# Optimization experiments

Hardware: AMD Instinct MI355X
Metric: run time of the kernel (lower is better)

## Reference

```python
import jax, jax.numpy as jnp
import numpy as np

N = 50000
E = 800000
D = 128
O = 128


def _spmm_coo(rows, cols, vals, x, n_rows):
    # out[r] += vals[e] * x[cols[e]]  (COO sparse matrix times dense matrix)
    gathered = vals[:, None] * x[cols]            # [E, O]
    return jax.ops.segment_sum(gathered, rows, num_segments=n_rows)


def setup_inputs() -> dict:
    key = jax.random.key(0)
    ks = jax.random.split(key, 9)
    return {
        "inputs": jax.random.normal(ks[0], (N, D), dtype=jnp.float32),
        "adj1_rows": jax.random.randint(ks[1], (E,), 0, N, dtype=jnp.int32),
        "adj1_cols": jax.random.randint(ks[2], (E,), 0, N, dtype=jnp.int32),
        "adj1_vals": jax.random.uniform(ks[3], (E,), dtype=jnp.float32),
        "adj2_rows": jax.random.randint(ks[4], (E,), 0, N, dtype=jnp.int32),
        "adj2_cols": jax.random.randint(ks[5], (E,), 0, N, dtype=jnp.int32),
        "adj2_vals": jax.random.uniform(ks[6], (E,), dtype=jnp.float32),
        "weights_1": jax.random.normal(ks[7], (D, O), dtype=jnp.float32) * (6.0 / (D + O)) ** 0.5,
        "weights_2": jax.random.normal(ks[8], (D, O), dtype=jnp.float32) * (6.0 / (D + O)) ** 0.5,
    }


def reference(inputs, adj1_rows, adj1_cols, adj1_vals,
              adj2_rows, adj2_cols, adj2_vals, weights_1, weights_2):
    # dense projection per relation
    x1 = inputs @ weights_1                        # [N, O]
    x2 = inputs @ weights_2                        # [N, O]
    # sparse aggregation per relation
    y1 = _spmm_coo(adj1_rows, adj1_cols, adj1_vals, x1, N)
    y2 = _spmm_coo(adj2_rows, adj2_cols, adj2_vals, x2, N)
    return jax.nn.relu(y1 + y2)
```

## Files before the change

kernel.cpp:

```cpp
#include <hip/hip_runtime.h>


typedef __attribute__((ext_vector_type(4))) float     f32x4;
typedef __attribute__((ext_vector_type(8))) short     bf16x8;

#define NB      782
#define BSLOTS  10
#define BCAP    2560
#define SCAP    64

static __device__ __forceinline__ unsigned short f2bf(float f) {
    unsigned u = __float_as_uint(f);
    u += 0x7FFF + ((u >> 16) & 1);
    return (unsigned short)(u >> 16);
}

__global__ __launch_bounds__(256) void convert_kernel(
    const float* __restrict__ X,
    const float* __restrict__ W1, const float* __restrict__ W2,
    unsigned short* __restrict__ Xb, unsigned short* __restrict__ Wt, int n)
{
    const int stride = gridDim.x * blockDim.x;
    const int nW = 2 * 128 * 128;
    const int nX = n * 32;
    const int total = nW + nX;
    for (int g = blockIdx.x * blockDim.x + threadIdx.x; g < total; g += stride) {
        if (g < nW) {
            const int rel = g >> 14;
            const int o   = (g >> 7) & 127;
            const int k   = g & 127;
            const float* W = rel ? W2 : W1;
            Wt[g] = f2bf(W[k * 128 + o]);
        } else {
            const int i = g - nW;
            const float4 v = ((const float4*)X)[i];
            ushort4 b;
            b.x = f2bf(v.x); b.y = f2bf(v.y); b.z = f2bf(v.z); b.w = f2bf(v.w);
            ((ushort4*)Xb)[i] = b;
        }
    }
}

__global__ __launch_bounds__(256) void bin_kernel(
    const int* __restrict__ rows1, const int* __restrict__ cols1, const float* __restrict__ vals1,
    const int* __restrict__ rows2, const int* __restrict__ cols2, const float* __restrict__ vals2,
    int* __restrict__ gcur, unsigned long long* __restrict__ edges_tmp,
    int E, int n)
{
    __shared__ unsigned long long stage[NB][BSLOTS];
    __shared__ int scnt[NB];

    for (int i = threadIdx.x; i < NB; i += 256) scnt[i] = 0;
    __syncthreads();

    const int stride = gridDim.x * 256;
    const int total  = 2 * E;
    for (int g = blockIdx.x * 256 + threadIdx.x; g < total; g += stride) {
        int r, col, rel; float v;
        if (g < E) { r = rows1[g]; col = cols1[g]; rel = 0; v = vals1[g]; }
        else       { int e = g - E; r = rows2[e]; col = cols2[e]; rel = 1; v = vals2[e]; }

        const int b = r >> 6;
        const unsigned lo = (unsigned)(r & 63) | ((unsigned)rel << 6) | ((unsigned)col << 7);
        const unsigned long long pack =
            (unsigned long long)lo | ((unsigned long long)__float_as_uint(v) << 32);

        const int pos = atomicAdd(&scnt[b], 1);
        if (pos < BSLOTS) {
            stage[b][pos] = pack;
        } else {
            int gp = atomicAdd(&gcur[b], 1);
            if (gp < BCAP) edges_tmp[(size_t)b * BCAP + gp] = pack;
        }
    }
    __syncthreads();

    for (int b = threadIdx.x; b < NB; b += 256) {
        int k = scnt[b]; if (k > BSLOTS) k = BSLOTS;
        if (k > 0) {
            int base = atomicAdd(&gcur[b], k);
            for (int i = 0; i < k; ++i)
                if (base + i < BCAP)
                    edges_tmp[(size_t)b * BCAP + base + i] = stage[b][i];
        }
    }
}

__global__ __launch_bounds__(256) void agg_kernel(
    const int* __restrict__ gcur,
    const unsigned long long* __restrict__ edges_tmp,
    const unsigned short* __restrict__ Xb,
    unsigned short* __restrict__ agg, int n)
{
    __shared__ unsigned long long lists[32 * SCAP];
    __shared__ int cnt[32];

    const int nwg = NB * 4;
    const int xcd = blockIdx.x & 7, bi = blockIdx.x >> 3;
    const int q8 = nwg >> 3;
    const int swz = xcd * q8 + bi;

    const int b   = swz >> 2;
    const int q   = swz & 3;
    const int tid = threadIdx.x;
    const int rowbase = b * 64 + q * 16;
    if (rowbase >= n) return;

    int sz = gcur[b]; if (sz > BCAP) sz = BCAP;
    const unsigned long long* ebase = edges_tmp + (size_t)b * BCAP;

    if (tid < 32) cnt[tid] = 0;
    __syncthreads();

    for (int e = tid; e < sz; e += 256) {
        const unsigned long long p = ebase[e];
        const unsigned lo = (unsigned)p;
        const int rl = (int)(lo & 63u);
        if ((rl >> 4) == q) {
            const int seg = ((rl & 15) << 1) | ((lo >> 6) & 1);
            const int pos = atomicAdd(&cnt[seg], 1);
            if (pos < SCAP) lists[seg * SCAP + pos] = p;
        }
    }
    __syncthreads();

    const int lane = tid & 31;
    const int grp  = tid >> 5;
    for (int seg = grp; seg < 32; seg += 8) {
        const int row = rowbase + (seg >> 1);
        if (row >= n) continue;
        const int rel = seg & 1;
        int m = cnt[seg]; if (m > SCAP) m = SCAP;
        const unsigned long long* lst = &lists[seg * SCAP];
        float4 acc = make_float4(0.f, 0.f, 0.f, 0.f);

        int e = 0;
        for (; e + 4 <= m; e += 4) {
            const unsigned long long p0 = lst[e + 0];
            const unsigned long long p1 = lst[e + 1];
            const unsigned long long p2 = lst[e + 2];
            const unsigned long long p3 = lst[e + 3];
            const ushort4 x0 = *(const ushort4*)&Xb[(size_t)(((unsigned)p0 >> 7) & 0xFFFFu) * 128 + lane * 4];
            const ushort4 x1 = *(const ushort4*)&Xb[(size_t)(((unsigned)p1 >> 7) & 0xFFFFu) * 128 + lane * 4];
            const ushort4 x2 = *(const ushort4*)&Xb[(size_t)(((unsigned)p2 >> 7) & 0xFFFFu) * 128 + lane * 4];
            const ushort4 x3 = *(const ushort4*)&Xb[(size_t)(((unsigned)p3 >> 7) & 0xFFFFu) * 128 + lane * 4];
            const float v0 = __uint_as_float((unsigned)(p0 >> 32));
            const float v1 = __uint_as_float((unsigned)(p1 >> 32));
            const float v2 = __uint_as_float((unsigned)(p2 >> 32));
            const float v3 = __uint_as_float((unsigned)(p3 >> 32));
            acc.x = fmaf(v0, __uint_as_float((unsigned)x0.x << 16), acc.x);
            acc.y = fmaf(v0, __uint_as_float((unsigned)x0.y << 16), acc.y);
            acc.z = fmaf(v0, __uint_as_float((unsigned)x0.z << 16), acc.z);
            acc.w = fmaf(v0, __uint_as_float((unsigned)x0.w << 16), acc.w);
            acc.x = fmaf(v1, __uint_as_float((unsigned)x1.x << 16), acc.x);
            acc.y = fmaf(v1, __uint_as_float((unsigned)x1.y << 16), acc.y);
            acc.z = fmaf(v1, __uint_as_float((unsigned)x1.z << 16), acc.z);
            acc.w = fmaf(v1, __uint_as_float((unsigned)x1.w << 16), acc.w);
            acc.x = fmaf(v2, __uint_as_float((unsigned)x2.x << 16), acc.x);
            acc.y = fmaf(v2, __uint_as_float((unsigned)x2.y << 16), acc.y);
            acc.z = fmaf(v2, __uint_as_float((unsigned)x2.z << 16), acc.z);
            acc.w = fmaf(v2, __uint_as_float((unsigned)x2.w << 16), acc.w);
            acc.x = fmaf(v3, __uint_as_float((unsigned)x3.x << 16), acc.x);
            acc.y = fmaf(v3, __uint_as_float((unsigned)x3.y << 16), acc.y);
            acc.z = fmaf(v3, __uint_as_float((unsigned)x3.z << 16), acc.z);
            acc.w = fmaf(v3, __uint_as_float((unsigned)x3.w << 16), acc.w);
        }
        for (; e < m; ++e) {
            const unsigned long long p = lst[e];
            const ushort4 xv = *(const ushort4*)&Xb[(size_t)(((unsigned)p >> 7) & 0xFFFFu) * 128 + lane * 4];
            const float v  = __uint_as_float((unsigned)(p >> 32));
            acc.x = fmaf(v, __uint_as_float((unsigned)xv.x << 16), acc.x);
            acc.y = fmaf(v, __uint_as_float((unsigned)xv.y << 16), acc.y);
            acc.z = fmaf(v, __uint_as_float((unsigned)xv.z << 16), acc.z);
            acc.w = fmaf(v, __uint_as_float((unsigned)xv.w << 16), acc.w);
        }

        ushort4 o;
        o.x = f2bf(acc.x); o.y = f2bf(acc.y); o.z = f2bf(acc.z); o.w = f2bf(acc.w);
        *(ushort4*)&agg[((size_t)rel * n + row) * 128 + lane * 4] = o;
    }
}

__global__ __launch_bounds__(256) void gemm_relu_kernel(
    const unsigned short* __restrict__ agg,
    const unsigned short* __restrict__ Wt,
    float* __restrict__ out, int n)
{
    const int lane = threadIdx.x & 63;
    const int w    = threadIdx.x >> 6;
    const int colbase = w * 32;
    const int l15 = lane & 15;
    const int lhi = lane >> 4;

    bf16x8 bfrag[2][2][4];
    #pragma unroll
    for (int rel = 0; rel < 2; ++rel) {
        const unsigned short* Wr = Wt + rel * 16384;
        #pragma unroll
        for (int ct = 0; ct < 2; ++ct) {
            const int o = colbase + ct * 16 + l15;
            #pragma unroll
            for (int ks = 0; ks < 4; ++ks)
                bfrag[rel][ct][ks] = *(const bf16x8*)&Wr[o * 128 + ks * 32 + lhi * 8];
        }
    }

    const int row0 = blockIdx.x * 32;
    const f32x4 zero = {0.f, 0.f, 0.f, 0.f};

    #pragma unroll
    for (int rt = 0; rt < 2; ++rt) {
        const int r0 = row0 + rt * 16;
        int ra = r0 + l15; if (ra >= n) ra = n - 1;
        bf16x8 af0[4], af1[4];
        #pragma unroll
        for (int ks = 0; ks < 4; ++ks) {
            af0[ks] = *(const bf16x8*)&agg[(size_t)ra * 128 + ks * 32 + lhi * 8];
            af1[ks] = *(const bf16x8*)&agg[((size_t)n + ra) * 128 + ks * 32 + lhi * 8];
        }

        f32x4 acc[2];
        acc[0] = zero; acc[1] = zero;
        #pragma unroll
        for (int ks = 0; ks < 4; ++ks) {
            acc[0] = __builtin_amdgcn_mfma_f32_16x16x32_bf16(af0[ks], bfrag[0][0][ks], acc[0], 0, 0, 0);
            acc[1] = __builtin_amdgcn_mfma_f32_16x16x32_bf16(af0[ks], bfrag[0][1][ks], acc[1], 0, 0, 0);
            acc[0] = __builtin_amdgcn_mfma_f32_16x16x32_bf16(af1[ks], bfrag[1][0][ks], acc[0], 0, 0, 0);
            acc[1] = __builtin_amdgcn_mfma_f32_16x16x32_bf16(af1[ks], bfrag[1][1][ks], acc[1], 0, 0, 0);
        }

        #pragma unroll
        for (int ct = 0; ct < 2; ++ct) {
            const int col = colbase + ct * 16 + l15;
            #pragma unroll
            for (int j = 0; j < 4; ++j) {
                const int r = r0 + lhi * 4 + j;
                if (r < n) out[(size_t)r * 128 + col] = fmaxf(acc[ct][j], 0.f);
            }
        }
    }
}

extern "C" void kernel_launch(void* const* d_in, const int* in_sizes, int n_in,
                              void* d_out, int out_size, void* d_ws, size_t ws_size,
                              hipStream_t stream)
{
    const float* X  = (const float*)d_in[0];
    const int*   r1 = (const int*)  d_in[1];
    const int*   c1 = (const int*)  d_in[2];
    const float* v1 = (const float*)d_in[3];
    const int*   r2 = (const int*)  d_in[4];
    const int*   c2 = (const int*)  d_in[5];
    const float* v2 = (const float*)d_in[6];
    const float* W1 = (const float*)d_in[7];
    const float* W2 = (const float*)d_in[8];
    float*       out = (float*)d_out;

    const int n = in_sizes[0] / 128;
    const int E = in_sizes[1];

    unsigned short* agg = (unsigned short*)d_ws;
    unsigned short* Xb  = agg + (size_t)2 * n * 128;
    unsigned short* Wt  = Xb + (size_t)n * 128;
    unsigned long long* edges_tmp =
        (unsigned long long*)(((uintptr_t)(Wt + 2 * 128 * 128) + 255) & ~(uintptr_t)255);
    int* gcur = (int*)(edges_tmp + (size_t)NB * BCAP);

    hipMemsetAsync(gcur, 0, NB * sizeof(int), stream);

    convert_kernel<<<2048, 256, 0, stream>>>(X, W1, W2, Xb, Wt, n);

    bin_kernel<<<512, 256, 0, stream>>>(r1, c1, v1, r2, c2, v2, gcur, edges_tmp, E, n);

    agg_kernel<<<NB * 4, 256, 0, stream>>>(gcur, edges_tmp, Xb, agg, n);

    gemm_relu_kernel<<<(n + 31) / 32, 256, 0, stream>>>(agg, Wt, out, n);
}
```

Baseline: 129.8 us.

## Two-pass radix binning of edges, fused convert, and persistent atomic-queue aggregation

Replaces the single-pass binning into 782 row buckets with two passes. The first pass buckets edges into 13 super-bins of 4096 rows, with relation 0 filling from the front and relation 1 from the back of each region, and it shares one launch with the bf16 conversion. A second kernel then splits each super-bin into 64-row buckets through larger shared-memory staging. This is meant to cut the global atomics and scattered writes caused by tiny per-block staging. The aggregation kernel becomes persistent and takes 16-row chunks from a global atomic counter. This adds an extra pass over the edge list and reuses the agg workspace as scratch for the super-bins.

```diff
diff --git a/kernel.cpp b/kernel.cpp
--- a/kernel.cpp
+++ b/kernel.cpp
@@ -5,9 +5,14 @@
 typedef __attribute__((ext_vector_type(8))) short     bf16x8;
 
 #define NB      782
-#define BSLOTS  10
+#define NSUP    13
+#define SB1     64
+#define SCAPS   147456
+#define B2BLK   79
 #define BCAP    2560
 #define SCAP    64
+#define BIN1G   2048
+#define CONVG   256
 
 static __device__ __forceinline__ unsigned short f2bf(float f) {
     unsigned u = __float_as_uint(f);
@@ -15,169 +20,248 @@
     return (unsigned short)(u >> 16);
 }
 
-__global__ __launch_bounds__(256) void convert_kernel(
+__global__ __launch_bounds__(256) void convbin1_kernel(
     const float* __restrict__ X,
     const float* __restrict__ W1, const float* __restrict__ W2,
-    unsigned short* __restrict__ Xb, unsigned short* __restrict__ Wt, int n)
-{
-    const int stride = gridDim.x * blockDim.x;
-    const int nW = 2 * 128 * 128;
-    const int nX = n * 32;
-    const int total = nW + nX;
-    for (int g = blockIdx.x * blockDim.x + threadIdx.x; g < total; g += stride) {
-        if (g < nW) {
-            const int rel = g >> 14;
-            const int o   = (g >> 7) & 127;
-            const int k   = g & 127;
-            const float* W = rel ? W2 : W1;
-            Wt[g] = f2bf(W[k * 128 + o]);
-        } else {
-            const int i = g - nW;
-            const float4 v = ((const float4*)X)[i];
-            ushort4 b;
-            b.x = f2bf(v.x); b.y = f2bf(v.y); b.z = f2bf(v.z); b.w = f2bf(v.w);
-            ((ushort4*)Xb)[i] = b;
-        }
-    }
-}
-
-__global__ __launch_bounds__(256) void bin_kernel(
     const int* __restrict__ rows1, const int* __restrict__ cols1, const float* __restrict__ vals1,
     const int* __restrict__ rows2, const int* __restrict__ cols2, const float* __restrict__ vals2,
-    int* __restrict__ gcur, unsigned long long* __restrict__ edges_tmp,
+    unsigned short* __restrict__ Xb, unsigned short* __restrict__ Wt,
+    int* __restrict__ gcur1, unsigned long long* __restrict__ super_tmp,
     int E, int n)
 {
-    __shared__ unsigned long long stage[NB][BSLOTS];
-    __shared__ int scnt[NB];
-
-    for (int i = threadIdx.x; i < NB; i += 256) scnt[i] = 0;
+    if (blockIdx.x >= BIN1G) {
+        const int stride = CONVG * 256;
+        const int nW = 2 * 128 * 128;
+        const int nX = n * 32;
+        const int total = nW + nX;
+        for (int g = (blockIdx.x - BIN1G) * 256 + threadIdx.x; g < total; g += stride) {
+            if (g < nW) {
+                const int rel = g >> 14;
+                const int o   = (g >> 7) & 127;
+                const int k   = g & 127;
+                const float* W = rel ? W2 : W1;
+                Wt[g] = f2bf(W[k * 128 + o]);
+            } else {
+                const int i = g - nW;
+                const float4 v = ((const float4*)X)[i];
+                ushort4 b;
+                b.x = f2bf(v.x); b.y = f2bf(v.y); b.z = f2bf(v.z); b.w = f2bf(v.w);
+                ((ushort4*)Xb)[i] = b;
+            }
+        }
+        return;
+    }
+
+    __shared__ unsigned long long stage[2 * NSUP][SB1];
+    __shared__ int scnt[2 * NSUP];
+
+    for (int i = threadIdx.x; i < 2 * NSUP; i += 256) scnt[i] = 0;
     __syncthreads();
 
-    const int stride = gridDim.x * 256;
-    const int total  = 2 * E;
-    for (int g = blockIdx.x * 256 + threadIdx.x; g < total; g += stride) {
+    const int total = 2 * E;
+    for (int g = blockIdx.x * 256 + threadIdx.x; g < total; g += BIN1G * 256) {
         int r, col, rel; float v;
         if (g < E) { r = rows1[g]; col = cols1[g]; rel = 0; v = vals1[g]; }
         else       { int e = g - E; r = rows2[e]; col = cols2[e]; rel = 1; v = vals2[e]; }
 
-        const int b = r >> 6;
-        const unsigned lo = (unsigned)(r & 63) | ((unsigned)rel << 6) | ((unsigned)col << 7);
+        const int s   = r >> 12;
+        const int key = s * 2 + rel;
         const unsigned long long pack =
-            (unsigned long long)lo | ((unsigned long long)__float_as_uint(v) << 32);
-
-        const int pos = atomicAdd(&scnt[b], 1);
-        if (pos < BSLOTS) {
-            stage[b][pos] = pack;
+            (unsigned long long)((unsigned)(r & 0xFFFF) | ((unsigned)col << 16))
+            | ((unsigned long long)__float_as_uint(v) << 32);
+
+        const int pos = atomicAdd(&scnt[key], 1);
+        if (pos < SB1) {
+            stage[key][pos] = pack;
         } else {
-            int gp = atomicAdd(&gcur[b], 1);
-            if (gp < BCAP) edges_tmp[(size_t)b * BCAP + gp] = pack;
+            if (rel == 0) {
+                int gp = atomicAdd(&gcur1[2 * s], 1);
+                if (gp < SCAPS) super_tmp[(size_t)s * SCAPS + gp] = pack;
+            } else {
+                int gp = atomicAdd(&gcur1[2 * s + 1], 1);
+                if (gp < SCAPS) super_tmp[(size_t)s * SCAPS + (SCAPS - 1 - gp)] = pack;
+            }
         }
     }
     __syncthreads();
 
-    for (int b = threadIdx.x; b < NB; b += 256) {
-        int k = scnt[b]; if (k > BSLOTS) k = BSLOTS;
+    for (int key = threadIdx.x; key < 2 * NSUP; key += 256) {
+        int k = scnt[key]; if (k > SB1) k = SB1;
         if (k > 0) {
-            int base = atomicAdd(&gcur[b], k);
-            for (int i = 0; i < k; ++i)
-                if (base + i < BCAP)
-                    edges_tmp[(size_t)b * BCAP + base + i] = stage[b][i];
-        }
+            const int s = key >> 1, rel = key & 1;
+            if (rel == 0) {
+                int base = atomicAdd(&gcur1[2 * s], k);
+                for (int i = 0; i < k; ++i) {
+                    int gp = base + i;
+                    if (gp < SCAPS) super_tmp[(size_t)s * SCAPS + gp] = stage[key][i];
+                }
+            } else {
+                int base = atomicAdd(&gcur1[2 * s + 1], k);
+                for (int i = 0; i < k; ++i) {
+                    int gp = base + i;
+                    if (gp < SCAPS) super_tmp[(size_t)s * SCAPS + (SCAPS - 1 - gp)] = stage[key][i];
+                }
+            }
+        }
+    }
+}
+
+__global__ __launch_bounds__(256) void bin2_kernel(
+    const int* __restrict__ gcur1,
+    const unsigned long long* __restrict__ super_tmp,
+    int* __restrict__ gcur2, unsigned long long* __restrict__ edges_tmp,
+    int n)
+{
+    __shared__ unsigned long long stage[64][32];
+    __shared__ int scnt[64];
+
+    const int s  = blockIdx.x / B2BLK;
+    const int bi = blockIdx.x % B2BLK;
+    const int tid = threadIdx.x;
+
+    for (int i = tid; i < 64; i += 256) scnt[i] = 0;
+    __syncthreads();
+
+    int lo = gcur1[2 * s];     if (lo > SCAPS) lo = SCAPS;
+    int hi = gcur1[2 * s + 1]; if (hi > SCAPS) hi = SCAPS;
+    const unsigned long long* reg = super_tmp + (size_t)s * SCAPS;
+
+    #pragma unroll
+    for (int rel = 0; rel < 2; ++rel) {
+        const int cnt = rel ? hi : lo;
+        for (int k = bi * 256 + tid; k < cnt; k += B2BLK * 256) {
+            const unsigned long long p = rel ? reg[SCAPS - 1 - k] : reg[k];
+            const unsigned lo32 = (unsigned)p;
+            const int row = (int)(lo32 & 0xFFFFu);
+            const int col = (int)(lo32 >> 16);
+            const unsigned long long pack =
+                (unsigned long long)((unsigned)(row & 63) | ((unsigned)rel << 6) | ((unsigned)col << 7))
+                | (p & 0xFFFFFFFF00000000ull);
+
+            const int bl  = (row >> 6) & 63;
+            const int pos = atomicAdd(&scnt[bl], 1);
+            if (pos < 32) {
+                stage[bl][pos] = pack;
+            } else {
+                const int b = row >> 6;
+                int gp = atomicAdd(&gcur2[b], 1);
+                if (gp < BCAP) edges_tmp[(size_t)b * BCAP + gp] = pack;
+            }
+        }
+        __syncthreads();
+        for (int bl = tid; bl < 64; bl += 256) {
+            int k = scnt[bl]; if (k > 32) k = 32;
+            if (k > 0) {
+                const int b = (s << 6) + bl;
+                int base = atomicAdd(&gcur2[b], k);
+                for (int i = 0; i < k; ++i)
+                    if (base + i < BCAP)
+                        edges_tmp[(size_t)b * BCAP + base + i] = stage[bl][i];
+            }
+            scnt[bl] = 0;
+        }
+        __syncthreads();
     }
 }
 
 __global__ __launch_bounds__(256) void agg_kernel(
-    const int* __restrict__ gcur,
+    const int* __restrict__ gcur2,
     const unsigned long long* __restrict__ edges_tmp,
     const unsigned short* __restrict__ Xb,
-    unsigned short* __restrict__ agg, int n)
+    unsigned short* __restrict__ agg,
+    int* __restrict__ wctr, int n)
 {
     __shared__ unsigned long long lists[32 * SCAP];
     __shared__ int cnt[32];
-
-    const int nwg = NB * 4;
-    const int xcd = blockIdx.x & 7, bi = blockIdx.x >> 3;
-    const int q8 = nwg >> 3;
-    const int swz = xcd * q8 + bi;
-
-    const int b   = swz >> 2;
-    const int q   = swz & 3;
+    __shared__ int chunk_s;
+
     const int tid = threadIdx.x;
-    const int rowbase = b * 64 + q * 16;
-    if (rowbase >= n) return;
-
-    int sz = gcur[b]; if (sz > BCAP) sz = BCAP;
-    const unsigned long long* ebase = edges_tmp + (size_t)b * BCAP;
-
-    if (tid < 32) cnt[tid] = 0;
-    __syncthreads();
-
-    for (int e = tid; e < sz; e += 256) {
-        const unsigned long long p = ebase[e];
-        const unsigned lo = (unsigned)p;
-        const int rl = (int)(lo & 63u);
-        if ((rl >> 4) == q) {
-            const int seg = ((rl & 15) << 1) | ((lo >> 6) & 1);
-            const int pos = atomicAdd(&cnt[seg], 1);
-            if (pos < SCAP) lists[seg * SCAP + pos] = p;
-        }
-    }
-    __syncthreads();
-
-    const int lane = tid & 31;
-    const int grp  = tid >> 5;
-    for (int seg = grp; seg < 32; seg += 8) {
-        const int row = rowbase + (seg >> 1);
-        if (row >= n) continue;
-        const int rel = seg & 1;
-        int m = cnt[seg]; if (m > SCAP) m = SCAP;
-        const unsigned long long* lst = &lists[seg * SCAP];
-        float4 acc = make_float4(0.f, 0.f, 0.f, 0.f);
-
-        int e = 0;
-        for (; e + 4 <= m; e += 4) {
-            const unsigned long long p0 = lst[e + 0];
-            const unsigned long long p1 = lst[e + 1];
-            const unsigned long long p2 = lst[e + 2];
-            const unsigned long long p3 = lst[e + 3];
-            const ushort4 x0 = *(const ushort4*)&Xb[(size_t)(((unsigned)p0 >> 7) & 0xFFFFu) * 128 + lane * 4];
-            const ushort4 x1 = *(const ushort4*)&Xb[(size_t)(((unsigned)p1 >> 7) & 0xFFFFu) * 128 + lane * 4];
-            const ushort4 x2 = *(const ushort4*)&Xb[(size_t)(((unsigned)p2 >> 7) & 0xFFFFu) * 128 + lane * 4];
-            const ushort4 x3 = *(const ushort4*)&Xb[(size_t)(((unsigned)p3 >> 7) & 0xFFFFu) * 128 + lane * 4];
-            const float v0 = __uint_as_float((unsigned)(p0 >> 32));
-            const float v1 = __uint_as_float((unsigned)(p1 >> 32));
-            const float v2 = __uint_as_float((unsigned)(p2 >> 32));
-            const float v3 = __uint_as_float((unsigned)(p3 >> 32));
-            acc.x = fmaf(v0, __uint_as_float((unsigned)x0.x << 16), acc.x);
-            acc.y = fmaf(v0, __uint_as_float((unsigned)x0.y << 16), acc.y);
-            acc.z = fmaf(v0, __uint_as_float((unsigned)x0.z << 16), acc.z);
-            acc.w = fmaf(v0, __uint_as_float((unsigned)x0.w << 16), acc.w);
-            acc.x = fmaf(v1, __uint_as_float((unsigned)x1.x << 16), acc.x);
-            acc.y = fmaf(v1, __uint_as_float((unsigned)x1.y << 16), acc.y);
-            acc.z = fmaf(v1, __uint_as_float((unsigned)x1.z << 16), acc.z);
-            acc.w = fmaf(v1, __uint_as_float((unsigned)x1.w << 16), acc.w);
-            acc.x = fmaf(v2, __uint_as_float((unsigned)x2.x << 16), acc.x);
-            acc.y = fmaf(v2, __uint_as_float((unsigned)x2.y << 16), acc.y);
-            acc.z = fmaf(v2, __uint_as_float((unsigned)x2.z << 16), acc.z);
-            acc.w = fmaf(v2, __uint_as_float((unsigned)x2.w << 16), acc.w);
-            acc.x = fmaf(v3, __uint_as_float((unsigned)x3.x << 16), acc.x);
-            acc.y = fmaf(v3, __uint_as_float((unsigned)x3.y << 16), acc.y);
-            acc.z = fmaf(v3, __uint_as_float((unsigned)x3.z << 16), acc.z);
-            acc.w = fmaf(v3, __uint_as_float((unsigned)x3.w << 16), acc.w);
-        }
-        for (; e < m; ++e) {
-            const unsigned long long p = lst[e];
-            const ushort4 xv = *(const ushort4*)&Xb[(size_t)(((unsigned)p >> 7) & 0xFFFFu) * 128 + lane * 4];
-            const float v  = __uint_as_float((unsigned)(p >> 32));
-            acc.x = fmaf(v, __uint_as_float((unsigned)xv.x << 16), acc.x);
-            acc.y = fmaf(v, __uint_as_float((unsigned)xv.y << 16), acc.y);
-            acc.z = fmaf(v, __uint_as_float((unsigned)xv.z << 16), acc.z);
-            acc.w = fmaf(v, __uint_as_float((unsigned)xv.w << 16), acc.w);
-        }
-
-        ushort4 o;
-        o.x = f2bf(acc.x); o.y = f2bf(acc.y); o.z = f2bf(acc.z); o.w = f2bf(acc.w);
-        *(ushort4*)&agg[((size_t)rel * n + row) * 128 + lane * 4] = o;
+    const int NQ = (n + 15) >> 4;
+
+    for (;;) {
+        __syncthreads();
+        if (tid == 0) chunk_s = atomicAdd(wctr, 1);
+        __syncthreads();
+        const int c = chunk_s;
+        if (c >= NQ) return;
+
+        const int b = c >> 2;
+        const int q = c & 3;
+        const int rowbase = c * 16;
+
+        int sz = gcur2[b]; if (sz > BCAP) sz = BCAP;
+        const unsigned long long* ebase = edges_tmp + (size_t)b * BCAP;
+
+        if (tid < 32) cnt[tid] = 0;
+        __syncthreads();
+
+        for (int e = tid; e < sz; e += 256) {
+            const unsigned long long p = ebase[e];
+            const unsigned lo = (unsigned)p;
+            const int rl = (int)(lo & 63u);
+            if ((rl >> 4) == q) {
+                const int seg = ((rl & 15) << 1) | ((lo >> 6) & 1);
+                const int pos = atomicAdd(&cnt[seg], 1);
+                if (pos < SCAP) lists[seg * SCAP + pos] = p;
+            }
+        }
+        __syncthreads();
+
+        const int lane = tid & 31;
+        const int grp  = tid >> 5;
+        for (int seg = grp; seg < 32; seg += 8) {
+            const int row = rowbase + (seg >> 1);
+            if (row >= n) continue;
+            const int rel = seg & 1;
+            int m = cnt[seg]; if (m > SCAP) m = SCAP;
+            const unsigned long long* lst = &lists[seg * SCAP];
+            float4 acc = make_float4(0.f, 0.f, 0.f, 0.f);
+
+            int e = 0;
+            for (; e + 4 <= m; e += 4) {
+                const unsigned long long p0 = lst[e + 0];
+                const unsigned long long p1 = lst[e + 1];
+                const unsigned long long p2 = lst[e + 2];
+                const unsigned long long p3 = lst[e + 3];
+                const ushort4 x0 = *(const ushort4*)&Xb[(size_t)(((unsigned)p0 >> 7) & 0xFFFFu) * 128 + lane * 4];
+                const ushort4 x1 = *(const ushort4*)&Xb[(size_t)(((unsigned)p1 >> 7) & 0xFFFFu) * 128 + lane * 4];
+                const ushort4 x2 = *(const ushort4*)&Xb[(size_t)(((unsigned)p2 >> 7) & 0xFFFFu) * 128 + lane * 4];
+                const ushort4 x3 = *(const ushort4*)&Xb[(size_t)(((unsigned)p3 >> 7) & 0xFFFFu) * 128 + lane * 4];
+                const float v0 = __uint_as_float((unsigned)(p0 >> 32));
+                const float v1 = __uint_as_float((unsigned)(p1 >> 32));
+                const float v2 = __uint_as_float((unsigned)(p2 >> 32));
+                const float v3 = __uint_as_float((unsigned)(p3 >> 32));
+                acc.x = fmaf(v0, __uint_as_float((unsigned)x0.x << 16), acc.x);
+                acc.y = fmaf(v0, __uint_as_float((unsigned)x0.y << 16), acc.y);
+                acc.z = fmaf(v0, __uint_as_float((unsigned)x0.z << 16), acc.z);
+                acc.w = fmaf(v0, __uint_as_float((unsigned)x0.w << 16), acc.w);
+                acc.x = fmaf(v1, __uint_as_float((unsigned)x1.x << 16), acc.x);
+                acc.y = fmaf(v1, __uint_as_float((unsigned)x1.y << 16), acc.y);
+                acc.z = fmaf(v1, __uint_as_float((unsigned)x1.z << 16), acc.z);
+                acc.w = fmaf(v1, __uint_as_float((unsigned)x1.w << 16), acc.w);
+                acc.x = fmaf(v2, __uint_as_float((unsigned)x2.x << 16), acc.x);
+                acc.y = fmaf(v2, __uint_as_float((unsigned)x2.y << 16), acc.y);
+                acc.z = fmaf(v2, __uint_as_float((unsigned)x2.z << 16), acc.z);
+                acc.w = fmaf(v2, __uint_as_float((unsigned)x2.w << 16), acc.w);
+                acc.x = fmaf(v3, __uint_as_float((unsigned)x3.x << 16), acc.x);
+                acc.y = fmaf(v3, __uint_as_float((unsigned)x3.y << 16), acc.y);
+                acc.z = fmaf(v3, __uint_as_float((unsigned)x3.z << 16), acc.z);
+                acc.w = fmaf(v3, __uint_as_float((unsigned)x3.w << 16), acc.w);
+            }
+            for (; e < m; ++e) {
+                const unsigned long long p = lst[e];
+                const ushort4 xv = *(const ushort4*)&Xb[(size_t)(((unsigned)p >> 7) & 0xFFFFu) * 128 + lane * 4];
+                const float v  = __uint_as_float((unsigned)(p >> 32));
+                acc.x = fmaf(v, __uint_as_float((unsigned)xv.x << 16), acc.x);
+                acc.y = fmaf(v, __uint_as_float((unsigned)xv.y << 16), acc.y);
+                acc.z = fmaf(v, __uint_as_float((unsigned)xv.z << 16), acc.z);
+                acc.w = fmaf(v, __uint_as_float((unsigned)xv.w << 16), acc.w);
+            }
+
+            ushort4 o;
+            o.x = f2bf(acc.x); o.y = f2bf(acc.y); o.z = f2bf(acc.z); o.w = f2bf(acc.w);
+            *(ushort4*)&agg[((size_t)rel * n + row) * 128 + lane * 4] = o;
+        }
     }
 }
 
@@ -260,19 +344,23 @@
     const int E = in_sizes[1];
 
     unsigned short* agg = (unsigned short*)d_ws;
+    unsigned long long* super_tmp = (unsigned long long*)d_ws;
     unsigned short* Xb  = agg + (size_t)2 * n * 128;
     unsigned short* Wt  = Xb + (size_t)n * 128;
     unsigned long long* edges_tmp =
         (unsigned long long*)(((uintptr_t)(Wt + 2 * 128 * 128) + 255) & ~(uintptr_t)255);
-    int* gcur = (int*)(edges_tmp + (size_t)NB * BCAP);
-
-    hipMemsetAsync(gcur, 0, NB * sizeof(int), stream);
-
-    convert_kernel<<<2048, 256, 0, stream>>>(X, W1, W2, Xb, Wt, n);
-
-    bin_kernel<<<512, 256, 0, stream>>>(r1, c1, v1, r2, c2, v2, gcur, edges_tmp, E, n);
-
-    agg_kernel<<<NB * 4, 256, 0, stream>>>(gcur, edges_tmp, Xb, agg, n);
+    int* gcur1 = (int*)(edges_tmp + (size_t)NB * BCAP);
+    int* gcur2 = gcur1 + 2 * NSUP;
+    int* wctr  = gcur2 + NB;
+
+    hipMemsetAsync(gcur1, 0, (2 * NSUP + NB + 1) * sizeof(int), stream);
+
+    convbin1_kernel<<<BIN1G + CONVG, 256, 0, stream>>>(
+        X, W1, W2, r1, c1, v1, r2, c2, v2, Xb, Wt, gcur1, super_tmp, E, n);
+
+    bin2_kernel<<<NSUP * B2BLK, 256, 0, stream>>>(gcur1, super_tmp, gcur2, edges_tmp, n);
+
+    agg_kernel<<<2048, 256, 0, stream>>>(gcur2, edges_tmp, Xb, agg, wctr, n);
 
     gemm_relu_kernel<<<(n + 31) / 32, 256, 0, stream>>>(agg, Wt, out, n);
 }
```

Result: slower. 194.8 us (+50.1%).

## Fuse convert and bin kernels, split bins by half, shrink agg tiles to 8 rows

Applied to the files above, without the earlier changes.

Merges the bf16 conversion and edge binning into one launch, where dedicated blocks do the conversion while the rest bin edges. The binning blocks now work in pairs: each pair reads a contiguous slice of edges and each block keeps only rows in its half of the bins, which halves shared staging per block and allows more staging slots. The aggregation kernel now processes 8 rows per workgroup instead of 16, doubling the grid, with an XCD-aware swizzle that handles a remainder. The intent is to overlap conversion with binning, drop a launch, and raise parallelism in aggregation, at the cost of each edge being read twice and more redundant bin scans in aggregation.

```diff
diff --git a/kernel.cpp b/kernel.cpp
--- a/kernel.cpp
+++ b/kernel.cpp
@@ -5,9 +5,12 @@
 typedef __attribute__((ext_vector_type(8))) short     bf16x8;
 
 #define NB      782
-#define BSLOTS  10
+#define NBH     391
+#define BSLOTS  12
 #define BCAP    2560
 #define SCAP    64
+#define BING    512
+#define CONVG   256
 
 static __device__ __forceinline__ unsigned short f2bf(float f) {
     unsigned u = __float_as_uint(f);
@@ -15,59 +18,70 @@
     return (unsigned short)(u >> 16);
 }
 
-__global__ __launch_bounds__(256) void convert_kernel(
+__global__ __launch_bounds__(256) void convbin_kernel(
     const float* __restrict__ X,
     const float* __restrict__ W1, const float* __restrict__ W2,
-    unsigned short* __restrict__ Xb, unsigned short* __restrict__ Wt, int n)
-{
-    const int stride = gridDim.x * blockDim.x;
-    const int nW = 2 * 128 * 128;
-    const int nX = n * 32;
-    const int total = nW + nX;
-    for (int g = blockIdx.x * blockDim.x + threadIdx.x; g < total; g += stride) {
-        if (g < nW) {
-            const int rel = g >> 14;
-            const int o   = (g >> 7) & 127;
-            const int k   = g & 127;
-            const float* W = rel ? W2 : W1;
-            Wt[g] = f2bf(W[k * 128 + o]);
-        } else {
-            const int i = g - nW;
-            const float4 v = ((const float4*)X)[i];
-            ushort4 b;
-            b.x = f2bf(v.x); b.y = f2bf(v.y); b.z = f2bf(v.z); b.w = f2bf(v.w);
-            ((ushort4*)Xb)[i] = b;
-        }
-    }
-}
-
-__global__ __launch_bounds__(256) void bin_kernel(
     const int* __restrict__ rows1, const int* __restrict__ cols1, const float* __restrict__ vals1,
     const int* __restrict__ rows2, const int* __restrict__ cols2, const float* __restrict__ vals2,
+    unsigned short* __restrict__ Xb, unsigned short* __restrict__ Wt,
     int* __restrict__ gcur, unsigned long long* __restrict__ edges_tmp,
     int E, int n)
 {
-    __shared__ unsigned long long stage[NB][BSLOTS];
-    __shared__ int scnt[NB];
-
-    for (int i = threadIdx.x; i < NB; i += 256) scnt[i] = 0;
-    __syncthreads();
-
-    const int stride = gridDim.x * 256;
-    const int total  = 2 * E;
-    for (int g = blockIdx.x * 256 + threadIdx.x; g < total; g += stride) {
+    if (blockIdx.x >= BING) {
+        const int stride = CONVG * 256;
+        const int nW = 2 * 128 * 128;
+        const int nX = n * 32;
+        const int total = nW + nX;
+        for (int g = (blockIdx.x - BING) * 256 + threadIdx.x; g < total; g += stride) {
+            if (g < nW) {
+                const int rel = g >> 14;
+                const int o   = (g >> 7) & 127;
+                const int k   = g & 127;
+                const float* W = rel ? W2 : W1;
+                Wt[g] = f2bf(W[k * 128 + o]);
+            } else {
+                const int i = g - nW;
+                const float4 v = ((const float4*)X)[i];
+                ushort4 b;
+                b.x = f2bf(v.x); b.y = f2bf(v.y); b.z = f2bf(v.z); b.w = f2bf(v.w);
+                ((ushort4*)Xb)[i] = b;
+            }
+        }
+        return;
+    }
+
+    __shared__ unsigned long long stage[NBH][BSLOTS];
+    __shared__ int scnt[NBH];
+
+    const int slice = blockIdx.x >> 1;
+    const int half  = blockIdx.x & 1;
+    const int tid   = threadIdx.x;
+
+    for (int i = tid; i < NBH; i += 256) scnt[i] = 0;
+    __syncthreads();
+
+    const int total = 2 * E;
+    const int per   = (total + (BING / 2) - 1) / (BING / 2);
+    const int base  = slice * per;
+    const int end   = min(base + per, total);
+
+    for (int g = base + tid; g < end; g += 256) {
         int r, col, rel; float v;
         if (g < E) { r = rows1[g]; col = cols1[g]; rel = 0; v = vals1[g]; }
         else       { int e = g - E; r = rows2[e]; col = cols2[e]; rel = 1; v = vals2[e]; }
 
-        const int b = r >> 6;
+        const int b  = r >> 6;
+        const int bh = (b >= NBH) ? 1 : 0;
+        if (bh != half) continue;
+
+        const int key = half ? b - NBH : b;
         const unsigned lo = (unsigned)(r & 63) | ((unsigned)rel << 6) | ((unsigned)col << 7);
         const unsigned long long pack =
             (unsigned long long)lo | ((unsigned long long)__float_as_uint(v) << 32);
 
-        const int pos = atomicAdd(&scnt[b], 1);
+        const int pos = atomicAdd(&scnt[key], 1);
         if (pos < BSLOTS) {
-            stage[b][pos] = pack;
+            stage[key][pos] = pack;
         } else {
             int gp = atomicAdd(&gcur[b], 1);
             if (gp < BCAP) edges_tmp[(size_t)b * BCAP + gp] = pack;
@@ -75,13 +89,14 @@
     }
     __syncthreads();
 
-    for (int b = threadIdx.x; b < NB; b += 256) {
-        int k = scnt[b]; if (k > BSLOTS) k = BSLOTS;
+    for (int key = tid; key < NBH; key += 256) {
+        int k = scnt[key]; if (k > BSLOTS) k = BSLOTS;
         if (k > 0) {
-            int base = atomicAdd(&gcur[b], k);
+            const int b = key + half * NBH;
+            int base2 = atomicAdd(&gcur[b], k);
             for (int i = 0; i < k; ++i)
-                if (base + i < BCAP)
-                    edges_tmp[(size_t)b * BCAP + base + i] = stage[b][i];
+                if (base2 + i < BCAP)
+                    edges_tmp[(size_t)b * BCAP + base2 + i] = stage[key][i];
         }
     }
 }
@@ -92,32 +107,34 @@
     const unsigned short* __restrict__ Xb,
     unsigned short* __restrict__ agg, int n)
 {
-    __shared__ unsigned long long lists[32 * SCAP];
-    __shared__ int cnt[32];
-
-    const int nwg = NB * 4;
-    const int xcd = blockIdx.x & 7, bi = blockIdx.x >> 3;
-    const int q8 = nwg >> 3;
-    const int swz = xcd * q8 + bi;
-
-    const int b   = swz >> 2;
-    const int q   = swz & 3;
+    __shared__ unsigned long long lists[16 * SCAP];
+    __shared__ int cnt[16];
+
+    const int NQ = (n + 7) >> 3;
+    const int orig = blockIdx.x;
+    const int xcd = orig & 7, bi = orig >> 3;
+    const int q8 = NQ >> 3, r8 = NQ & 7;
+    const int swz = (xcd < r8) ? xcd * (q8 + 1) + bi
+                               : r8 * (q8 + 1) + (xcd - r8) * q8 + bi;
+    if (swz >= NQ) return;
+
+    const int b   = swz >> 3;
+    const int oct = swz & 7;
+    const int rowbase = swz * 8;
     const int tid = threadIdx.x;
-    const int rowbase = b * 64 + q * 16;
-    if (rowbase >= n) return;
 
     int sz = gcur[b]; if (sz > BCAP) sz = BCAP;
     const unsigned long long* ebase = edges_tmp + (size_t)b * BCAP;
 
-    if (tid < 32) cnt[tid] = 0;
+    if (tid < 16) cnt[tid] = 0;
     __syncthreads();
 
     for (int e = tid; e < sz; e += 256) {
         const unsigned long long p = ebase[e];
         const unsigned lo = (unsigned)p;
         const int rl = (int)(lo & 63u);
-        if ((rl >> 4) == q) {
-            const int seg = ((rl & 15) << 1) | ((lo >> 6) & 1);
+        if ((rl >> 3) == oct) {
+            const int seg = ((rl & 7) << 1) | ((lo >> 6) & 1);
             const int pos = atomicAdd(&cnt[seg], 1);
             if (pos < SCAP) lists[seg * SCAP + pos] = p;
         }
@@ -126,7 +143,7 @@
 
     const int lane = tid & 31;
     const int grp  = tid >> 5;
-    for (int seg = grp; seg < 32; seg += 8) {
+    for (int seg = grp; seg < 16; seg += 8) {
         const int row = rowbase + (seg >> 1);
         if (row >= n) continue;
         const int rel = seg & 1;
@@ -268,11 +285,10 @@
 
     hipMemsetAsync(gcur, 0, NB * sizeof(int), stream);
 
-    convert_kernel<<<2048, 256, 0, stream>>>(X, W1, W2, Xb, Wt, n);
-
-    bin_kernel<<<512, 256, 0, stream>>>(r1, c1, v1, r2, c2, v2, gcur, edges_tmp, E, n);
-
-    agg_kernel<<<NB * 4, 256, 0, stream>>>(gcur, edges_tmp, Xb, agg, n);
+    convbin_kernel<<<BING + CONVG, 256, 0, stream>>>(
+        X, W1, W2, r1, c1, v1, r2, c2, v2, Xb, Wt, gcur, edges_tmp, E, n);
+
+    agg_kernel<<<(n + 7) / 8, 256, 0, stream>>>(gcur, edges_tmp, Xb, agg, n);
 
     gemm_relu_kernel<<<(n + 31) / 32, 256, 0, stream>>>(agg, Wt, out, n);
 }
```

Result: slower. 135.1 us (+4.1%).

## Sort bucket edges by row segment and split aggregation by column groups

Applied to the files above, without the earlier changes.

Adds a sort2 kernel that counting-sorts each bucket's edges by (row, relation) into contiguous segments with per-bucket segment pointers, replacing the per-block LDS list building with its SCAP overflow cap. The aggregation kernel now has each block handle one 32-column slice of a 64-row bucket, reading sorted edges directly from global memory, so blocks no longer rescan the whole bucket. The gcur memset is folded into convert_kernel. This adds an extra kernel launch and a global read/write pass over the edges, and narrows the per-lane gathers to 4-byte loads.

```diff
diff --git a/kernel.cpp b/kernel.cpp
--- a/kernel.cpp
+++ b/kernel.cpp
@@ -7,19 +7,26 @@
 #define NB      782
 #define BSLOTS  10
 #define BCAP    2560
-#define SCAP    64
+#define SPITCH  132
 
 static __device__ __forceinline__ unsigned short f2bf(float f) {
     unsigned u = __float_as_uint(f);
     u += 0x7FFF + ((u >> 16) & 1);
     return (unsigned short)(u >> 16);
 }
+static __device__ __forceinline__ float b2f(unsigned short s) {
+    return __uint_as_float((unsigned)s << 16);
+}
 
 __global__ __launch_bounds__(256) void convert_kernel(
     const float* __restrict__ X,
     const float* __restrict__ W1, const float* __restrict__ W2,
-    unsigned short* __restrict__ Xb, unsigned short* __restrict__ Wt, int n)
-{
+    unsigned short* __restrict__ Xb, unsigned short* __restrict__ Wt,
+    int* __restrict__ gcur, int n)
+{
+    if (blockIdx.x == 0)
+        for (int i = threadIdx.x; i < NB; i += 256) gcur[i] = 0;
+
     const int stride = gridDim.x * blockDim.x;
     const int nW = 2 * 128 * 128;
     const int nX = n * 32;
@@ -86,98 +93,121 @@
     }
 }
 
-__global__ __launch_bounds__(256) void agg_kernel(
+__global__ __launch_bounds__(256) void sort2_kernel(
     const int* __restrict__ gcur,
-    const unsigned long long* __restrict__ edges_tmp,
-    const unsigned short* __restrict__ Xb,
-    unsigned short* __restrict__ agg, int n)
-{
-    __shared__ unsigned long long lists[32 * SCAP];
-    __shared__ int cnt[32];
-
-    const int nwg = NB * 4;
-    const int xcd = blockIdx.x & 7, bi = blockIdx.x >> 3;
-    const int q8 = nwg >> 3;
-    const int swz = xcd * q8 + bi;
-
-    const int b   = swz >> 2;
-    const int q   = swz & 3;
+    unsigned long long* __restrict__ edges_tmp,
+    int* __restrict__ seg_ptr)
+{
+    __shared__ unsigned long long sout[BCAP];
+    __shared__ int hist[128];
+    __shared__ int ptr[129];
+    __shared__ int cur[128];
+
+    const int b   = blockIdx.x;
     const int tid = threadIdx.x;
-    const int rowbase = b * 64 + q * 16;
-    if (rowbase >= n) return;
-
     int sz = gcur[b]; if (sz > BCAP) sz = BCAP;
-    const unsigned long long* ebase = edges_tmp + (size_t)b * BCAP;
-
-    if (tid < 32) cnt[tid] = 0;
+    unsigned long long* ebase = edges_tmp + (size_t)b * BCAP;
+
+    if (tid < 128) hist[tid] = 0;
+    __syncthreads();
+
+    for (int e = tid; e < sz; e += 256) {
+        const unsigned lo = (unsigned)ebase[e];
+        atomicAdd(&hist[((lo & 63u) << 1) | ((lo >> 6) & 1)], 1);
+    }
+    __syncthreads();
+
+    if (tid < 128) {
+        int v = hist[tid], x = v;
+        #pragma unroll
+        for (int off = 1; off < 64; off <<= 1) {
+            int t = __shfl_up(x, off, 64);
+            if ((tid & 63) >= off) x += t;
+        }
+        ptr[tid + 1] = x;
+    }
+    if (tid == 0) ptr[0] = 0;
+    __syncthreads();
+    if (tid >= 64 && tid < 128) {
+        const int t = ptr[64];
+        ptr[tid + 1] += t;
+    }
+    __syncthreads();
+    if (tid < 128) cur[tid] = ptr[tid];
     __syncthreads();
 
     for (int e = tid; e < sz; e += 256) {
         const unsigned long long p = ebase[e];
         const unsigned lo = (unsigned)p;
-        const int rl = (int)(lo & 63u);
-        if ((rl >> 4) == q) {
-            const int seg = ((rl & 15) << 1) | ((lo >> 6) & 1);
-            const int pos = atomicAdd(&cnt[seg], 1);
-            if (pos < SCAP) lists[seg * SCAP + pos] = p;
-        }
-    }
-    __syncthreads();
-
-    const int lane = tid & 31;
-    const int grp  = tid >> 5;
-    for (int seg = grp; seg < 32; seg += 8) {
-        const int row = rowbase + (seg >> 1);
+        const int pos = atomicAdd(&cur[((lo & 63u) << 1) | ((lo >> 6) & 1)], 1);
+        sout[pos] = p;
+    }
+    __syncthreads();
+
+    for (int e = tid; e < sz; e += 256) ebase[e] = sout[e];
+    if (tid <= 128) seg_ptr[b * SPITCH + tid] = ptr[tid];
+}
+
+__global__ __launch_bounds__(256) void agg_kernel(
+    const unsigned long long* __restrict__ edges_tmp,
+    const int* __restrict__ seg_ptr,
+    const unsigned short* __restrict__ Xb,
+    unsigned short* __restrict__ agg, int n)
+{
+    const int tid  = threadIdx.x;
+    const int lane = tid & 15;
+    const int grp  = tid >> 4;
+
+    const int orig = blockIdx.x;
+    const int xcd  = orig & 7;
+    const int cg   = xcd >> 1;
+    const int b    = ((orig >> 3) << 1) | (xcd & 1);
+
+    const unsigned long long* ebase = edges_tmp + (size_t)b * BCAP;
+    const int* sptr = seg_ptr + b * SPITCH;
+    const int colbase = cg * 32 + lane * 2;
+
+    for (int s = grp; s < 128; s += 16) {
+        const int row = b * 64 + (s >> 1);
         if (row >= n) continue;
-        const int rel = seg & 1;
-        int m = cnt[seg]; if (m > SCAP) m = SCAP;
-        const unsigned long long* lst = &lists[seg * SCAP];
-        float4 acc = make_float4(0.f, 0.f, 0.f, 0.f);
-
-        int e = 0;
-        for (; e + 4 <= m; e += 4) {
-            const unsigned long long p0 = lst[e + 0];
-            const unsigned long long p1 = lst[e + 1];
-            const unsigned long long p2 = lst[e + 2];
-            const unsigned long long p3 = lst[e + 3];
-            const ushort4 x0 = *(const ushort4*)&Xb[(size_t)(((unsigned)p0 >> 7) & 0xFFFFu) * 128 + lane * 4];
-            const ushort4 x1 = *(const ushort4*)&Xb[(size_t)(((unsigned)p1 >> 7) & 0xFFFFu) * 128 + lane * 4];
-            const ushort4 x2 = *(const ushort4*)&Xb[(size_t)(((unsigned)p2 >> 7) & 0xFFFFu) * 128 + lane * 4];
-            const ushort4 x3 = *(const ushort4*)&Xb[(size_t)(((unsigned)p3 >> 7) & 0xFFFFu) * 128 + lane * 4];
+        const int rel = s & 1;
+        const int e0 = sptr[s], e1 = sptr[s + 1];
+
+        float ax = 0.f, ay = 0.f;
+        int e = e0;
+        for (; e + 4 <= e1; e += 4) {
+            const unsigned long long p0 = ebase[e + 0];
+            const unsigned long long p1 = ebase[e + 1];
+            const unsigned long long p2 = ebase[e + 2];
+            const unsigned long long p3 = ebase[e + 3];
+            const unsigned c0 = ((unsigned)p0 >> 7) & 0xFFFFu;
+            const unsigned c1 = ((unsigned)p1 >> 7) & 0xFFFFu;
+            const unsigned c2 = ((unsigned)p2 >> 7) & 0xFFFFu;
+            const unsigned c3 = ((unsigned)p3 >> 7) & 0xFFFFu;
+            const ushort2 x0 = *(const ushort2*)&Xb[(size_t)c0 * 128 + colbase];
+            const ushort2 x1 = *(const ushort2*)&Xb[(size_t)c1 * 128 + colbase];
+            const ushort2 x2 = *(const ushort2*)&Xb[(size_t)c2 * 128 + colbase];
+            const ushort2 x3 = *(const ushort2*)&Xb[(size_t)c3 * 128 + colbase];
             const float v0 = __uint_as_float((unsigned)(p0 >> 32));
             const float v1 = __uint_as_float((unsigned)(p1 >> 32));
             const float v2 = __uint_as_float((unsigned)(p2 >> 32));
             const float v3 = __uint_as_float((unsigned)(p3 >> 32));
-            acc.x = fmaf(v0, __uint_as_float((unsigned)x0.x << 16), acc.x);
-            acc.y = fmaf(v0, __uint_as_float((unsigned)x0.y << 16), acc.y);
-            acc.z = fmaf(v0, __uint_as_float((unsigned)x0.z << 16), acc.z);
-            acc.w = fmaf(v0, __uint_as_float((unsigned)x0.w << 16), acc.w);
-            acc.x = fmaf(v1, __uint_as_float((unsigned)x1.x << 16), acc.x);
-            acc.y = fmaf(v1, __uint_as_float((unsigned)x1.y << 16), acc.y);
-            acc.z = fmaf(v1, __uint_as_float((unsigned)x1.z << 16), acc.z);
-            acc.w = fmaf(v1, __uint_as_float((unsigned)x1.w << 16), acc.w);
-            acc.x = fmaf(v2, __uint_as_float((unsigned)x2.x << 16), acc.x);
-            acc.y = fmaf(v2, __uint_as_float((unsigned)x2.y << 16), acc.y);
-            acc.z = fmaf(v2, __uint_as_float((unsigned)x2.z << 16), acc.z);
-            acc.w = fmaf(v2, __uint_as_float((unsigned)x2.w << 16), acc.w);
-            acc.x = fmaf(v3, __uint_as_float((unsigned)x3.x << 16), acc.x);
-            acc.y = fmaf(v3, __uint_as_float((unsigned)x3.y << 16), acc.y);
-            acc.z = fmaf(v3, __uint_as_float((unsigned)x3.z << 16), acc.z);
-            acc.w = fmaf(v3, __uint_as_float((unsigned)x3.w << 16), acc.w);
-        }
-        for (; e < m; ++e) {
-            const unsigned long long p = lst[e];
-            const ushort4 xv = *(const ushort4*)&Xb[(size_t)(((unsigned)p >> 7) & 0xFFFFu) * 128 + lane * 4];
-            const float v  = __uint_as_float((unsigned)(p >> 32));
-            acc.x = fmaf(v, __uint_as_float((unsigned)xv.x << 16), acc.x);
-            acc.y = fmaf(v, __uint_as_float((unsigned)xv.y << 16), acc.y);
-            acc.z = fmaf(v, __uint_as_float((unsigned)xv.z << 16), acc.z);
-            acc.w = fmaf(v, __uint_as_float((unsigned)xv.w << 16), acc.w);
-        }
-
-        ushort4 o;
-        o.x = f2bf(acc.x); o.y = f2bf(acc.y); o.z = f2bf(acc.z); o.w = f2bf(acc.w);
-        *(ushort4*)&agg[((size_t)rel * n + row) * 128 + lane * 4] = o;
+            ax = fmaf(v0, b2f(x0.x), ax);  ay = fmaf(v0, b2f(x0.y), ay);
+            ax = fmaf(v1, b2f(x1.x), ax);  ay = fmaf(v1, b2f(x1.y), ay);
+            ax = fmaf(v2, b2f(x2.x), ax);  ay = fmaf(v2, b2f(x2.y), ay);
+            ax = fmaf(v3, b2f(x3.x), ax);  ay = fmaf(v3, b2f(x3.y), ay);
+        }
+        for (; e < e1; ++e) {
+            const unsigned long long p = ebase[e];
+            const unsigned c = ((unsigned)p >> 7) & 0xFFFFu;
+            const ushort2 xv = *(const ushort2*)&Xb[(size_t)c * 128 + colbase];
+            const float v = __uint_as_float((unsigned)(p >> 32));
+            ax = fmaf(v, b2f(xv.x), ax);  ay = fmaf(v, b2f(xv.y), ay);
+        }
+
+        ushort2 o;
+        o.x = f2bf(ax);  o.y = f2bf(ay);
+        *(ushort2*)&agg[((size_t)rel * n + row) * 128 + colbase] = o;
     }
 }
 
@@ -264,15 +294,16 @@
     unsigned short* Wt  = Xb + (size_t)n * 128;
     unsigned long long* edges_tmp =
         (unsigned long long*)(((uintptr_t)(Wt + 2 * 128 * 128) + 255) & ~(uintptr_t)255);
-    int* gcur = (int*)(edges_tmp + (size_t)NB * BCAP);
-
-    hipMemsetAsync(gcur, 0, NB * sizeof(int), stream);
-
-    convert_kernel<<<2048, 256, 0, stream>>>(X, W1, W2, Xb, Wt, n);
+    int* seg_ptr = (int*)(edges_tmp + (size_t)NB * BCAP);
+    int* gcur    = seg_ptr + NB * SPITCH;
+
+    convert_kernel<<<2048, 256, 0, stream>>>(X, W1, W2, Xb, Wt, gcur, n);
 
     bin_kernel<<<512, 256, 0, stream>>>(r1, c1, v1, r2, c2, v2, gcur, edges_tmp, E, n);
 
-    agg_kernel<<<NB * 4, 256, 0, stream>>>(gcur, edges_tmp, Xb, agg, n);
+    sort2_kernel<<<NB, 256, 0, stream>>>(gcur, edges_tmp, seg_ptr);
+
+    agg_kernel<<<NB * 4, 256, 0, stream>>>(edges_tmp, seg_ptr, Xb, agg, n);
 
     gemm_relu_kernel<<<(n + 31) / 32, 256, 0, stream>>>(agg, Wt, out, n);
 }
```

Measured after the change: 189.6 us. 1.46x slower.
